# Kernel optimization log

Measured on AMD Instinct MI355X. Metric: run time of the kernel, lower is better.

The kernel has to match this reference:

```python
import jax, jax.numpy as jnp
import numpy as np
import math

NUM_EMBED = 1024
EMBED_DIM = 256
COMMITMENT_COST = 0.25


def setup_inputs() -> dict:
    key = jax.random.key(0)
    k1, k2 = jax.random.split(key)
    inputs = jax.random.normal(k1, (16, EMBED_DIM, 4096), dtype=jnp.float32)
    embed = jax.random.normal(k2, (NUM_EMBED, EMBED_DIM), dtype=jnp.float32)
    return {"inputs": inputs, "embed": embed}


def reference(inputs, embed):
    sg = jax.lax.stop_gradient
    num_embed = embed.shape[0]
    # channels-first (B, D, T) -> (B, T, D)
    x = jnp.swapaxes(inputs, 1, -1)
    B, T, D = x.shape
    flat = x.reshape(-1, D)  # (N, D)
    # pairwise squared distances to the codebook: (N, K)
    d2 = (jnp.sum(flat * flat, axis=1, keepdims=True)
          + jnp.sum(embed * embed, axis=1)
          - 2.0 * flat @ embed.T)
    q_idx = jnp.argmin(d2, axis=1)  # (N,) int
    # one-hot @ embed is just a gather of the nearest codewords
    z_q = embed[q_idx].reshape(x.shape)  # (B, T, D)
    vq_loss = jnp.mean((z_q - sg(x)) ** 2)
    commitment_loss = jnp.mean((sg(z_q) - x) ** 2)
    loss = vq_loss + COMMITMENT_COST * commitment_loss
    # straight-through estimator
    z_q_st = x + sg(z_q - x)
    # codebook usage stats: probs = mean of the one-hot rows
    n = flat.shape[0]
    probs = jnp.zeros((num_embed,), dtype=flat.dtype).at[q_idx].add(1.0) / n
    perplexity = jnp.exp(-jnp.sum(probs * jnp.log(probs + 1e-10)))
    num_spatial_positions = n / B  # == T
    kldiv_r = (math.log(num_embed) * num_spatial_positions
               * jnp.ones((B, 1), dtype=x.dtype))
    z_q_out = jnp.swapaxes(z_q_st, 1, -1)  # back to (B, D, T)
    return z_q_out, loss, kldiv_r, perplexity
```

## Files before the change

### kernel.cpp

```cpp
#include <hip/hip_runtime.h>
#include <math.h>

#define T_DIM 4096
#define D_DIM 256
#define K_NUM 1024
#define B_NUM 16
#define N_TOT (B_NUM * T_DIM)
#define EPS_FLAG 0.25f

typedef float f32x4 __attribute__((ext_vector_type(4)));
typedef _Float16 half8 __attribute__((ext_vector_type(8)));

#define WS_FLAGCNT 0
#define WS_LOSS 4
#define WS_DONE 8
#define WS_HIST 64
#define WS_E2 4352
#define WS_QIDX 8704
#define WS_FLAGLIST 270848
#define WS_BESTD 532992
#define WS_ESWZ 795136
#define WS_ET4 1319424
#define WS_XROWS_ET 2368000
#define WS_XROWS_NOET 1319424

__device__ inline unsigned umin_(unsigned a, unsigned b) { return a < b ? a : b; }
__device__ inline unsigned umax_(unsigned a, unsigned b) { return a > b ? a : b; }

__global__ __launch_bounds__(256) void prep_kernel(const float* __restrict__ embed,
                                                   unsigned char* __restrict__ eswz,
                                                   float* __restrict__ e2,
                                                   float4* __restrict__ eT4, int useET,
                                                   int* __restrict__ wszero) {
    const int tid = threadIdx.x;
    if (blockIdx.x == 0) {
        #pragma unroll
        for (int i = tid; i < 1040; i += 256) wszero[i] = 0;
    }
    const int col = blockIdx.x * 8 + (tid >> 5);
    const int c = tid & 31;
    const float* src = embed + (size_t)col * D_DIM + c * 8;
    half8 h;
    float f[8];
    float s = 0.f;
    #pragma unroll
    for (int j = 0; j < 8; ++j) {
        float v = src[j];
        f[j] = v;
        h[j] = (_Float16)v;
        s = fmaf(v, v, s);
    }
    const int g = col >> 4;
    const int k = c >> 2;
    const int l = ((c & 3) << 4) | (col & 15);
    *(half8*)(eswz + (size_t)g * 8192 + k * 1024 + l * 16) = h;
    if (useET) {
        float4 a = {f[0], f[1], f[2], f[3]};
        float4 b = {f[4], f[5], f[6], f[7]};
        eT4[(size_t)(c * 2 + 0) * K_NUM + col] = a;
        eT4[(size_t)(c * 2 + 1) * K_NUM + col] = b;
    }
    #pragma unroll
    for (int off = 16; off; off >>= 1) s += __shfl_down(s, off);
    if ((tid & 31) == 0) e2[col] = s;
}

#define LOADB(BUF, P) do {                                                        \
    const unsigned char* _bp = eswz + (size_t)(P) * 8192 + (size_t)(l * 16);      \
    _Pragma("unroll")                                                             \
    for (int _k = 0; _k < 8; ++_k) BUF[_k] = *(const half8*)(_bp + _k * 1024);    \
} while (0)

#define PHASE(BUF, P) do {                                                                     \
    const float _bias = fmaf(e2s[(P) * 16 + (l & 15)], -0.5f, -1024.f);                        \
    f32x4 c0e = {_bias, _bias, _bias, _bias};                                                  \
    f32x4 c1e = {_bias, _bias, _bias, _bias};                                                  \
    f32x4 c0o = {0.f, 0.f, 0.f, 0.f};                                                          \
    f32x4 c1o = {0.f, 0.f, 0.f, 0.f};                                                          \
    c0e = __builtin_amdgcn_mfma_f32_16x16x32_f16(Ah[0][0], BUF[0], c0e, 0, 0, 0);              \
    c1e = __builtin_amdgcn_mfma_f32_16x16x32_f16(Ah[1][0], BUF[0], c1e, 0, 0, 0);              \
    c0o = __builtin_amdgcn_mfma_f32_16x16x32_f16(Ah[0][1], BUF[1], c0o, 0, 0, 0);              \
    c1o = __builtin_amdgcn_mfma_f32_16x16x32_f16(Ah[1][1], BUF[1], c1o, 0, 0, 0);              \
    c0e = __builtin_amdgcn_mfma_f32_16x16x32_f16(Ah[0][2], BUF[2], c0e, 0, 0, 0);              \
    c1e = __builtin_amdgcn_mfma_f32_16x16x32_f16(Ah[1][2], BUF[2], c1e, 0, 0, 0);              \
    c0o = __builtin_amdgcn_mfma_f32_16x16x32_f16(Ah[0][3], BUF[3], c0o, 0, 0, 0);              \
    c1o = __builtin_amdgcn_mfma_f32_16x16x32_f16(Ah[1][3], BUF[3], c1o, 0, 0, 0);              \
    c0e = __builtin_amdgcn_mfma_f32_16x16x32_f16(Ah[0][4], BUF[4], c0e, 0, 0, 0);              \
    c1e = __builtin_amdgcn_mfma_f32_16x16x32_f16(Ah[1][4], BUF[4], c1e, 0, 0, 0);              \
    c0o = __builtin_amdgcn_mfma_f32_16x16x32_f16(Ah[0][5], BUF[5], c0o, 0, 0, 0);              \
    c1o = __builtin_amdgcn_mfma_f32_16x16x32_f16(Ah[1][5], BUF[5], c1o, 0, 0, 0);              \
    c0e = __builtin_amdgcn_mfma_f32_16x16x32_f16(Ah[0][6], BUF[6], c0e, 0, 0, 0);              \
    c1e = __builtin_amdgcn_mfma_f32_16x16x32_f16(Ah[1][6], BUF[6], c1e, 0, 0, 0);              \
    c0o = __builtin_amdgcn_mfma_f32_16x16x32_f16(Ah[0][7], BUF[7], c0o, 0, 0, 0);              \
    c1o = __builtin_amdgcn_mfma_f32_16x16x32_f16(Ah[1][7], BUF[7], c1o, 0, 0, 0);              \
    const unsigned _tag = (unsigned)(P);                                                       \
    _Pragma("unroll")                                                                          \
    for (int _r = 0; _r < 4; ++_r) {                                                           \
        float d0v = (c0e[_r] + c0o[_r]) * -2.f;                                                \
        float d1v = (c1e[_r] + c1o[_r]) * -2.f;                                                \
        unsigned k0 = (__float_as_uint(d0v) & 0xFFFFFFC0u) | _tag;                             \
        unsigned k1 = (__float_as_uint(d1v) & 0xFFFFFFC0u) | _tag;                             \
        unsigned m0 = umax_(bestk[_r], k0);                                                    \
        bestk[_r] = umin_(bestk[_r], k0);                                                      \
        seck[_r] = umin_(seck[_r], m0);                                                        \
        unsigned m1 = umax_(bestk[4 + _r], k1);                                                \
        bestk[4 + _r] = umin_(bestk[4 + _r], k1);                                              \
        seck[4 + _r] = umin_(seck[4 + _r], m1);                                                \
    }                                                                                          \
} while (0)

__global__ __launch_bounds__(256, 2) void argmin_mfma_kernel(
    const float* __restrict__ x, const unsigned char* __restrict__ eswz,
    const float* __restrict__ e2, const float* __restrict__ embed,
    int* __restrict__ qidx, int* __restrict__ flagcnt, int* __restrict__ flaglist,
    float* __restrict__ bestd, float* __restrict__ xrows,
    float* __restrict__ out, int* __restrict__ hist,
    float* __restrict__ loss_sum, int cap)
{
    __shared__ float e2s[K_NUM];
    __shared__ __align__(16) float tile[64 * 128];
    __shared__ int   qid_lds[128];
    __shared__ int   lrows[128];
    __shared__ float lbest[128];
    __shared__ int   lcnt;
    __shared__ int   gbase;

    const int tid = threadIdx.x;
    const int w = tid >> 6;
    const int l = tid & 63;
    const int rb = blockIdx.x * 128;
    const int b = rb >> 12;
    const float* xb = x + (size_t)b * (D_DIM * T_DIM);
    if (tid == 0) lcnt = 0;

    half8 B0[8], B1[8];
    LOADB(B0, 0);

    for (int i = tid; i < K_NUM; i += 256) e2s[i] = e2[i];

    half8 Ah[2][8];
    float x2v[2];
    #pragma unroll
    for (int f = 0; f < 2; ++f) {
        const int row = rb + w * 32 + f * 16 + (l & 15);
        const int t = row & (T_DIM - 1);
        const float* xp = xb + t;
        float s2 = 0.f;
        #pragma unroll
        for (int k = 0; k < 8; ++k) {
            const int d0 = k * 32 + ((l >> 4) << 3);
            half8 h;
            #pragma unroll
            for (int j = 0; j < 8; ++j) {
                float v = xp[(size_t)(d0 + j) * T_DIM];
                h[j] = (_Float16)v;
                s2 = fmaf(v, v, s2);
            }
            Ah[f][k] = h;
        }
        x2v[f] = s2;
    }
    #pragma unroll
    for (int f = 0; f < 2; ++f) {
        x2v[f] += __shfl_xor(x2v[f], 16);
        x2v[f] += __shfl_xor(x2v[f], 32);
    }
    __syncthreads();

    unsigned bestk[8], seck[8];
    #pragma unroll
    for (int s = 0; s < 8; ++s) { bestk[s] = 0xFFFFFFFFu; seck[s] = 0xFFFFFFFFu; }

    for (int pp = 0; pp < 31; ++pp) {
        LOADB(B1, 2 * pp + 1);
        PHASE(B0, 2 * pp);
        LOADB(B0, 2 * pp + 2);
        PHASE(B1, 2 * pp + 1);
    }
    LOADB(B1, 63);
    PHASE(B0, 62);
    PHASE(B1, 63);

    float lossw = 0.f;
    #pragma unroll
    for (int slot = 0; slot < 8; ++slot) {
        float bv = __uint_as_float(bestk[slot] & 0xFFFFFFC0u) - 2048.f;
        float sv = __uint_as_float(seck[slot] & 0xFFFFFFC0u) - 2048.f;
        int bi = (int)(bestk[slot] & 63u) * 16 + (l & 15);
        #pragma unroll
        for (int d = 1; d < 16; d <<= 1) {
            float ob = __shfl_xor(bv, d);
            int   oi = __shfl_xor(bi, d);
            float os = __shfl_xor(sv, d);
            bool take = (ob < bv) || (ob == bv && oi < bi);
            float loser = take ? bv : ob;
            bv = take ? ob : bv;
            bi = take ? oi : bi;
            sv = fminf(fminf(sv, os), loser);
        }
        const int srcl = ((l >> 4) << 2) + (slot & 3);
        const float x2r = __shfl(x2v[slot >> 2], srcl);
        if ((l & 15) == 0) {
            const int rloc = w * 32 + (slot >> 2) * 16 + (l >> 4) * 4 + (slot & 3);
            qidx[rb + rloc] = bi;
            qid_lds[rloc] = bi;
            atomicAdd(&hist[bi], 1);
            lossw += bv + x2r;
            if (sv - bv < EPS_FLAG) {
                int lp = atomicAdd(&lcnt, 1);
                lrows[lp] = rb + rloc;
                lbest[lp] = bv;
            }
        }
    }
    lossw += __shfl_down(lossw, 16);
    lossw += __shfl_down(lossw, 32);
    if (l == 0) atomicAdd(loss_sum, lossw);

    __syncthreads();
    const int nloc = lcnt;
    if (tid == 0) gbase = nloc ? atomicAdd(flagcnt, nloc) : 0;
    __syncthreads();
    for (int i = w; i < nloc; i += 4) {
        const int row = lrows[i];
        const int p = gbase + i;
        const bool have = (p < cap);
        if (have) {
            const float* xp = xb + (row & (T_DIM - 1));
            float4 vv;
            vv.x = xp[(size_t)(l * 4 + 0) * T_DIM];
            vv.y = xp[(size_t)(l * 4 + 1) * T_DIM];
            vv.z = xp[(size_t)(l * 4 + 2) * T_DIM];
            vv.w = xp[(size_t)(l * 4 + 3) * T_DIM];
            *(float4*)(xrows + (size_t)p * D_DIM + l * 4) = vv;
        }
        if (l == 0) {
            flaglist[p] = have ? row : (row | 0x80000000);
            bestd[p] = lbest[i];
        }
    }

    const int t0 = rb & (T_DIM - 1);
    float* outb = out + (size_t)b * (D_DIM * T_DIM);
    for (int c = 0; c < 4; ++c) {
        const int d0 = c * 64;
        __syncthreads();
        {
            const int r = tid & 127;
            const int half = tid >> 7;
            const int qi = qid_lds[r];
            const float4* ep = (const float4*)(embed + (size_t)qi * D_DIM + d0 + half * 32);
            #pragma unroll
            for (int i = 0; i < 8; ++i) {
                const float4 ev = ep[i];
                const int dl = half * 32 + i * 4;
                tile[(dl + 0) * 128 + r] = ev.x;
                tile[(dl + 1) * 128 + r] = ev.y;
                tile[(dl + 2) * 128 + r] = ev.z;
                tile[(dl + 3) * 128 + r] = ev.w;
            }
        }
        __syncthreads();
        #pragma unroll 4
        for (int j = 0; j < 32; ++j) {
            const int flat = j * 256 + tid;
            const int dl = flat >> 7;
            const int rr = flat & 127;
            outb[(size_t)(d0 + dl) * T_DIM + t0 + rr] = tile[dl * 128 + rr];
        }
    }
}

__global__ __launch_bounds__(256) void cleanup_kernel(
    const float* __restrict__ x, const float* __restrict__ xrows,
    const float* __restrict__ embed, const float4* __restrict__ eT4, int useET,
    const float* __restrict__ e2,
    const int* __restrict__ flagcnt, const int* __restrict__ flaglist,
    int* __restrict__ qidx, const float* __restrict__ bestd,
    float* __restrict__ loss_sum, float* __restrict__ out, int* __restrict__ hist,
    int* __restrict__ donecnt)
{
    __shared__ float xr[8][256];
    __shared__ float rvall[8][256];
    __shared__ int   rixall[8][256];
    __shared__ int   rowss[8];
    __shared__ int   amlast;
    const int tid = threadIdx.x;
    const int w = tid >> 6;
    int cnt = flagcnt[0];
    if (cnt > N_TOT) cnt = N_TOT;
    for (int base = blockIdx.x * 8; base < cnt; base += gridDim.x * 8) {
        const int nr = (cnt - base < 8) ? (cnt - base) : 8;
        __syncthreads();
        if (tid < 8) rowss[tid] = (tid < nr) ? flaglist[base + tid] : 0;
        __syncthreads();
        #pragma unroll
        for (int r = 0; r < 8; ++r) {
            float v = 0.f;
            if (r < nr) {
                const int fe = rowss[r];
                if (fe >= 0) {
                    v = xrows[(size_t)(base + r) * D_DIM + tid];
                } else {
                    const int row = fe & 0x7FFFFFFF;
                    v = x[(size_t)(row >> 12) * (D_DIM * T_DIM) + (size_t)tid * T_DIM
                          + (row & (T_DIM - 1))];
                }
            }
            xr[r][tid] = v;
        }
        __syncthreads();

        float acc[4][8];
        #pragma unroll
        for (int q = 0; q < 4; ++q)
            #pragma unroll
            for (int r = 0; r < 8; ++r) acc[q][r] = 0.f;
        #pragma unroll 2
        for (int dd4 = 0; dd4 < 64; ++dd4) {
            float4 ev[4];
            #pragma unroll
            for (int q = 0; q < 4; ++q) {
                const int c = q * 256 + tid;
                ev[q] = useET ? eT4[(size_t)dd4 * K_NUM + c]
                              : *((const float4*)(embed + (size_t)c * D_DIM) + dd4);
            }
            float4 xv[8];
            #pragma unroll
            for (int r = 0; r < 8; ++r) xv[r] = *(const float4*)&xr[r][dd4 * 4];
            #pragma unroll
            for (int q = 0; q < 4; ++q) {
                #pragma unroll
                for (int r = 0; r < 8; ++r) {
                    acc[q][r] = fmaf(ev[q].x, xv[r].x, acc[q][r]);
                    acc[q][r] = fmaf(ev[q].y, xv[r].y, acc[q][r]);
                    acc[q][r] = fmaf(ev[q].z, xv[r].z, acc[q][r]);
                    acc[q][r] = fmaf(ev[q].w, xv[r].w, acc[q][r]);
                }
            }
        }
        float bv[8]; int bix[8];
        #pragma unroll
        for (int r = 0; r < 8; ++r) { bv[r] = 3.4e38f; bix[r] = 0x7FFFFFFF; }
        #pragma unroll
        for (int q = 0; q < 4; ++q) {
            const int c = q * 256 + tid;
            const float ec = e2[c];
            #pragma unroll
            for (int r = 0; r < 8; ++r) {
                const float s = fmaf(-2.f, acc[q][r], ec);
                if (s < bv[r] || (s == bv[r] && c < bix[r])) { bv[r] = s; bix[r] = c; }
            }
        }
        #pragma unroll
        for (int r = 0; r < 8; ++r) { rvall[r][tid] = bv[r]; rixall[r][tid] = bix[r]; }
        __syncthreads();
        const int ll = tid & 63;
        #pragma unroll
        for (int rr2 = 0; rr2 < 2; ++rr2) {
            const int r = w * 2 + rr2;
            float mv = 3.4e38f; int mi = 0x7FFFFFFF;
            #pragma unroll
            for (int j = 0; j < 4; ++j) {
                const float v = rvall[r][ll + j * 64];
                const int i2 = rixall[r][ll + j * 64];
                if (v < mv || (v == mv && i2 < mi)) { mv = v; mi = i2; }
            }
            #pragma unroll
            for (int d = 1; d < 64; d <<= 1) {
                const float ov = __shfl_xor(mv, d);
                const int   oi = __shfl_xor(mi, d);
                if (ov < mv || (ov == mv && oi < mi)) { mv = ov; mi = oi; }
            }
            if (r < nr) {
                const int row = rowss[r] & 0x7FFFFFFF;
                const int old = qidx[row];
                if (mi != old) {
                    const int b2 = row >> 12, t2 = row & (T_DIM - 1);
                    const float4 ev = *(const float4*)(embed + (size_t)mi * D_DIM + ll * 4);
                    float* op = out + (size_t)b2 * (D_DIM * T_DIM) + t2;
                    op[(size_t)(ll * 4 + 0) * T_DIM] = ev.x;
                    op[(size_t)(ll * 4 + 1) * T_DIM] = ev.y;
                    op[(size_t)(ll * 4 + 2) * T_DIM] = ev.z;
                    op[(size_t)(ll * 4 + 3) * T_DIM] = ev.w;
                    if (ll == 0) {
                        qidx[row] = mi;
                        atomicAdd(&hist[mi], 1);
                        atomicAdd(&hist[old], -1);
                    }
                }
                if (ll == 0) atomicAdd(loss_sum, mv - bestd[base + r]);
            }
        }
    }

    __threadfence();
    if (tid == 0) {
        const int old = atomicAdd(donecnt, 1);
        amlast = (old == (int)gridDim.x - 1) ? 1 : 0;
    }
    __syncthreads();
    if (amlast) {
        float acc = 0.f;
        for (int i = tid; i < K_NUM; i += 256) {
            const int h = __hip_atomic_load(&hist[i], __ATOMIC_RELAXED,
                                            __HIP_MEMORY_SCOPE_AGENT);
            const float p = (float)h * (1.f / (float)N_TOT);
            acc += p * logf(p + 1e-10f);
        }
        #pragma unroll
        for (int off = 32; off; off >>= 1) acc += __shfl_down(acc, off);
        __shared__ float ls[4];
        if ((tid & 63) == 0) ls[tid >> 6] = acc;
        __syncthreads();
        if (tid == 0) {
            const float H = -(ls[0] + ls[1] + ls[2] + ls[3]);
            const float L = __hip_atomic_load(loss_sum, __ATOMIC_RELAXED,
                                              __HIP_MEMORY_SCOPE_AGENT);
            const size_t base = (size_t)N_TOT * D_DIM;
            out[base] = 1.25f * L * (1.f / 16777216.f);
            const float kld = (float)(6.931471805599453 * 4096.0);
            #pragma unroll
            for (int i = 0; i < 16; ++i) out[base + 1 + i] = kld;
            out[base + 17] = expf(H);
        }
    }
}

extern "C" void kernel_launch(void* const* d_in, const int* in_sizes, int n_in,
                              void* d_out, int out_size, void* d_ws, size_t ws_size,
                              hipStream_t stream)
{
    const float* x     = (const float*)d_in[0];
    const float* embed = (const float*)d_in[1];
    float* out = (float*)d_out;

    char* ws = (char*)d_ws;
    int*   flagcnt  = (int*)(ws + WS_FLAGCNT);
    float* loss_sum = (float*)(ws + WS_LOSS);
    int*   donecnt  = (int*)(ws + WS_DONE);
    int*   hist     = (int*)(ws + WS_HIST);
    float* e2       = (float*)(ws + WS_E2);
    int*   qidx     = (int*)(ws + WS_QIDX);
    int*   flaglist = (int*)(ws + WS_FLAGLIST);
    float* bestd    = (float*)(ws + WS_BESTD);
    unsigned char* eswz = (unsigned char*)(ws + WS_ESWZ);
    float4* eT4     = (float4*)(ws + WS_ET4);

    const int useET = (ws_size >= (size_t)WS_XROWS_ET + 2048) ? 1 : 0;
    const size_t xrows_off = useET ? (size_t)WS_XROWS_ET : (size_t)WS_XROWS_NOET;
    float* xrows = (float*)(ws + xrows_off);

    int cap = 0;
    if (ws_size > xrows_off + 1024) {
        size_t c = (ws_size - xrows_off) / 1024;
        cap = (c > (size_t)N_TOT) ? N_TOT : (int)c;
    }

    prep_kernel<<<128, 256, 0, stream>>>(embed, eswz, e2, eT4, useET, (int*)ws);
    argmin_mfma_kernel<<<N_TOT / 128, 256, 0, stream>>>(x, eswz, e2, embed, qidx,
                                                        flagcnt, flaglist, bestd, xrows,
                                                        out, hist, loss_sum, cap);
    cleanup_kernel<<<512, 256, 0, stream>>>(x, xrows, embed, eT4, useET, e2,
                                            flagcnt, flaglist, qidx, bestd,
                                            loss_sum, out, hist, donecnt);
}
```

Measured before the change: 269.2 us.

## Triple-buffer codebook loads, drop the per-distance scaling, add nontemporal x loads and stores

The MFMA argmin loop moves from double to triple buffering of the swizzled codebook fragments, so loads for a phase are issued further ahead of the MFMAs that consume them. The per-element multiply by -2 is removed. The kernel now tracks a maximum of the positive biased dot-product key, and the distance is rebuilt only once after the loop. The input reads and the output stores become nontemporal to reduce cache pollution. The extra 32 VGPRs for the third buffer could cause spills or lower occupancy under launch_bounds(256,2), and ties between equal keys now resolve to the higher tag.

```diff
diff --git a/kernel.cpp b/kernel.cpp
--- a/kernel.cpp
+++ b/kernel.cpp
@@ -72,7 +72,7 @@
 } while (0)
 
 #define PHASE(BUF, P) do {                                                                     \
-    const float _bias = fmaf(e2s[(P) * 16 + (l & 15)], -0.5f, -1024.f);                        \
+    const float _bias = fmaf(e2s[(P) * 16 + (l & 15)], -0.5f, 1024.f);                         \
     f32x4 c0e = {_bias, _bias, _bias, _bias};                                                  \
     f32x4 c1e = {_bias, _bias, _bias, _bias};                                                  \
     f32x4 c0o = {0.f, 0.f, 0.f, 0.f};                                                          \
@@ -96,16 +96,16 @@
     const unsigned _tag = (unsigned)(P);                                                       \
     _Pragma("unroll")                                                                          \
     for (int _r = 0; _r < 4; ++_r) {                                                           \
-        float d0v = (c0e[_r] + c0o[_r]) * -2.f;                                                \
-        float d1v = (c1e[_r] + c1o[_r]) * -2.f;                                                \
-        unsigned k0 = (__float_as_uint(d0v) & 0xFFFFFFC0u) | _tag;                             \
-        unsigned k1 = (__float_as_uint(d1v) & 0xFFFFFFC0u) | _tag;                             \
-        unsigned m0 = umax_(bestk[_r], k0);                                                    \
-        bestk[_r] = umin_(bestk[_r], k0);                                                      \
-        seck[_r] = umin_(seck[_r], m0);                                                        \
-        unsigned m1 = umax_(bestk[4 + _r], k1);                                                \
-        bestk[4 + _r] = umin_(bestk[4 + _r], k1);                                              \
-        seck[4 + _r] = umin_(seck[4 + _r], m1);                                                \
+        float m0v = c0e[_r] + c0o[_r];                                                         \
+        float m1v = c1e[_r] + c1o[_r];                                                         \
+        unsigned k0 = (__float_as_uint(m0v) & 0xFFFFFFC0u) | _tag;                             \
+        unsigned k1 = (__float_as_uint(m1v) & 0xFFFFFFC0u) | _tag;                             \
+        unsigned d0 = umin_(bestk[_r], k0);                                                    \
+        bestk[_r] = umax_(bestk[_r], k0);                                                      \
+        seck[_r] = umax_(seck[_r], d0);                                                        \
+        unsigned d1 = umin_(bestk[4 + _r], k1);                                                \
+        bestk[4 + _r] = umax_(bestk[4 + _r], k1);                                              \
+        seck[4 + _r] = umax_(seck[4 + _r], d1);                                                \
     }                                                                                          \
 } while (0)
 
@@ -133,8 +133,10 @@
     const float* xb = x + (size_t)b * (D_DIM * T_DIM);
     if (tid == 0) lcnt = 0;
 
-    half8 B0[8], B1[8];
+    half8 B0[8], B1[8], B2[8];
     LOADB(B0, 0);
+    LOADB(B1, 1);
+    LOADB(B2, 2);
 
     for (int i = tid; i < K_NUM; i += 256) e2s[i] = e2[i];
 
@@ -152,7 +154,7 @@
             half8 h;
             #pragma unroll
             for (int j = 0; j < 8; ++j) {
-                float v = xp[(size_t)(d0 + j) * T_DIM];
+                float v = __builtin_nontemporal_load(xp + (size_t)(d0 + j) * T_DIM);
                 h[j] = (_Float16)v;
                 s2 = fmaf(v, v, s2);
             }
@@ -169,23 +171,25 @@
 
     unsigned bestk[8], seck[8];
     #pragma unroll
-    for (int s = 0; s < 8; ++s) { bestk[s] = 0xFFFFFFFFu; seck[s] = 0xFFFFFFFFu; }
-
-    for (int pp = 0; pp < 31; ++pp) {
-        LOADB(B1, 2 * pp + 1);
-        PHASE(B0, 2 * pp);
-        LOADB(B0, 2 * pp + 2);
-        PHASE(B1, 2 * pp + 1);
-    }
-    LOADB(B1, 63);
-    PHASE(B0, 62);
-    PHASE(B1, 63);
+    for (int s = 0; s < 8; ++s) { bestk[s] = 0u; seck[s] = 0u; }
+
+    for (int pp = 0; pp < 20; ++pp) {
+        PHASE(B0, 3 * pp);     LOADB(B0, 3 * pp + 3);
+        PHASE(B1, 3 * pp + 1); LOADB(B1, 3 * pp + 4);
+        PHASE(B2, 3 * pp + 2); LOADB(B2, 3 * pp + 5);
+    }
+    PHASE(B0, 60); LOADB(B0, 63);
+    PHASE(B1, 61);
+    PHASE(B2, 62);
+    PHASE(B0, 63);
 
     float lossw = 0.f;
     #pragma unroll
     for (int slot = 0; slot < 8; ++slot) {
-        float bv = __uint_as_float(bestk[slot] & 0xFFFFFFC0u) - 2048.f;
-        float sv = __uint_as_float(seck[slot] & 0xFFFFFFC0u) - 2048.f;
+        const float mBf = __uint_as_float(bestk[slot] & 0xFFFFFFC0u);
+        const float mSf = __uint_as_float(seck[slot] & 0xFFFFFFC0u);
+        float bv = fmaf(-2.f, mBf, 2048.f);
+        float sv = fmaf(-2.f, mSf, 2048.f);
         int bi = (int)(bestk[slot] & 63u) * 16 + (l & 15);
         #pragma unroll
         for (int d = 1; d < 16; d <<= 1) {
@@ -266,7 +270,8 @@
             const int flat = j * 256 + tid;
             const int dl = flat >> 7;
             const int rr = flat & 127;
-            outb[(size_t)(d0 + dl) * T_DIM + t0 + rr] = tile[dl * 128 + rr];
+            __builtin_nontemporal_store(tile[dl * 128 + rr],
+                                        &outb[(size_t)(d0 + dl) * T_DIM + t0 + rr]);
         }
     }
 }
```

Result: slower. 286.9 us (+6.6%).

## Halve rows per wave in argmin kernel, raise occupancy, flip to max-key tracking

Applied to the files above, without the earlier changes.

Each wave now handles 16 rows instead of 32, so the block covers 64 rows and the grid doubles, while launch bounds ask for 4 blocks per CU instead of 2. The distance is rewritten as a positive score (1024 + x·e − e2/2) and tracked with unsigned max, removing the per-element multiply by -2 and half the accumulator and best/second registers. Codebook B-fragments are preloaded one phase further ahead. This lowers register pressure to gain occupancy and latency hiding, at the cost of loading the codebook from L2 twice as often per row.

```diff
diff --git a/kernel.cpp b/kernel.cpp
--- a/kernel.cpp
+++ b/kernel.cpp
@@ -72,44 +72,29 @@
 } while (0)
 
 #define PHASE(BUF, P) do {                                                                     \
-    const float _bias = fmaf(e2s[(P) * 16 + (l & 15)], -0.5f, -1024.f);                        \
-    f32x4 c0e = {_bias, _bias, _bias, _bias};                                                  \
-    f32x4 c1e = {_bias, _bias, _bias, _bias};                                                  \
-    f32x4 c0o = {0.f, 0.f, 0.f, 0.f};                                                          \
-    f32x4 c1o = {0.f, 0.f, 0.f, 0.f};                                                          \
-    c0e = __builtin_amdgcn_mfma_f32_16x16x32_f16(Ah[0][0], BUF[0], c0e, 0, 0, 0);              \
-    c1e = __builtin_amdgcn_mfma_f32_16x16x32_f16(Ah[1][0], BUF[0], c1e, 0, 0, 0);              \
-    c0o = __builtin_amdgcn_mfma_f32_16x16x32_f16(Ah[0][1], BUF[1], c0o, 0, 0, 0);              \
-    c1o = __builtin_amdgcn_mfma_f32_16x16x32_f16(Ah[1][1], BUF[1], c1o, 0, 0, 0);              \
-    c0e = __builtin_amdgcn_mfma_f32_16x16x32_f16(Ah[0][2], BUF[2], c0e, 0, 0, 0);              \
-    c1e = __builtin_amdgcn_mfma_f32_16x16x32_f16(Ah[1][2], BUF[2], c1e, 0, 0, 0);              \
-    c0o = __builtin_amdgcn_mfma_f32_16x16x32_f16(Ah[0][3], BUF[3], c0o, 0, 0, 0);              \
-    c1o = __builtin_amdgcn_mfma_f32_16x16x32_f16(Ah[1][3], BUF[3], c1o, 0, 0, 0);              \
-    c0e = __builtin_amdgcn_mfma_f32_16x16x32_f16(Ah[0][4], BUF[4], c0e, 0, 0, 0);              \
-    c1e = __builtin_amdgcn_mfma_f32_16x16x32_f16(Ah[1][4], BUF[4], c1e, 0, 0, 0);              \
-    c0o = __builtin_amdgcn_mfma_f32_16x16x32_f16(Ah[0][5], BUF[5], c0o, 0, 0, 0);              \
-    c1o = __builtin_amdgcn_mfma_f32_16x16x32_f16(Ah[1][5], BUF[5], c1o, 0, 0, 0);              \
-    c0e = __builtin_amdgcn_mfma_f32_16x16x32_f16(Ah[0][6], BUF[6], c0e, 0, 0, 0);              \
-    c1e = __builtin_amdgcn_mfma_f32_16x16x32_f16(Ah[1][6], BUF[6], c1e, 0, 0, 0);              \
-    c0o = __builtin_amdgcn_mfma_f32_16x16x32_f16(Ah[0][7], BUF[7], c0o, 0, 0, 0);              \
-    c1o = __builtin_amdgcn_mfma_f32_16x16x32_f16(Ah[1][7], BUF[7], c1o, 0, 0, 0);              \
+    const float _bias = fmaf(e2s[(P) * 16 + (l & 15)], -0.5f, 1024.f);                         \
+    f32x4 ce = {_bias, _bias, _bias, _bias};                                                   \
+    f32x4 co = {0.f, 0.f, 0.f, 0.f};                                                          \
+    ce = __builtin_amdgcn_mfma_f32_16x16x32_f16(Ah[0], BUF[0], ce, 0, 0, 0);                   \
+    co = __builtin_amdgcn_mfma_f32_16x16x32_f16(Ah[1], BUF[1], co, 0, 0, 0);                   \
+    ce = __builtin_amdgcn_mfma_f32_16x16x32_f16(Ah[2], BUF[2], ce, 0, 0, 0);                   \
+    co = __builtin_amdgcn_mfma_f32_16x16x32_f16(Ah[3], BUF[3], co, 0, 0, 0);                   \
+    ce = __builtin_amdgcn_mfma_f32_16x16x32_f16(Ah[4], BUF[4], ce, 0, 0, 0);                   \
+    co = __builtin_amdgcn_mfma_f32_16x16x32_f16(Ah[5], BUF[5], co, 0, 0, 0);                   \
+    ce = __builtin_amdgcn_mfma_f32_16x16x32_f16(Ah[6], BUF[6], ce, 0, 0, 0);                   \
+    co = __builtin_amdgcn_mfma_f32_16x16x32_f16(Ah[7], BUF[7], co, 0, 0, 0);                   \
     const unsigned _tag = (unsigned)(P);                                                       \
     _Pragma("unroll")                                                                          \
     for (int _r = 0; _r < 4; ++_r) {                                                           \
-        float d0v = (c0e[_r] + c0o[_r]) * -2.f;                                                \
-        float d1v = (c1e[_r] + c1o[_r]) * -2.f;                                                \
-        unsigned k0 = (__float_as_uint(d0v) & 0xFFFFFFC0u) | _tag;                             \
-        unsigned k1 = (__float_as_uint(d1v) & 0xFFFFFFC0u) | _tag;                             \
-        unsigned m0 = umax_(bestk[_r], k0);                                                    \
-        bestk[_r] = umin_(bestk[_r], k0);                                                      \
-        seck[_r] = umin_(seck[_r], m0);                                                        \
-        unsigned m1 = umax_(bestk[4 + _r], k1);                                                \
-        bestk[4 + _r] = umin_(bestk[4 + _r], k1);                                              \
-        seck[4 + _r] = umin_(seck[4 + _r], m1);                                                \
+        float mv = ce[_r] + co[_r];                                                            \
+        unsigned kk = (__float_as_uint(mv) & 0xFFFFFFC0u) | _tag;                              \
+        unsigned dd = umin_(bestk[_r], kk);                                                    \
+        bestk[_r] = umax_(bestk[_r], kk);                                                      \
+        seck[_r] = umax_(seck[_r], dd);                                                        \
     }                                                                                          \
 } while (0)
 
-__global__ __launch_bounds__(256, 2) void argmin_mfma_kernel(
+__global__ __launch_bounds__(256, 4) void argmin_mfma_kernel(
     const float* __restrict__ x, const unsigned char* __restrict__ eswz,
     const float* __restrict__ e2, const float* __restrict__ embed,
     int* __restrict__ qidx, int* __restrict__ flagcnt, int* __restrict__ flaglist,
@@ -118,31 +103,31 @@
     float* __restrict__ loss_sum, int cap)
 {
     __shared__ float e2s[K_NUM];
-    __shared__ __align__(16) float tile[64 * 128];
-    __shared__ int   qid_lds[128];
-    __shared__ int   lrows[128];
-    __shared__ float lbest[128];
+    __shared__ __align__(16) float tile[64 * 64];
+    __shared__ int   qid_lds[64];
+    __shared__ int   lrows[64];
+    __shared__ float lbest[64];
     __shared__ int   lcnt;
     __shared__ int   gbase;
 
     const int tid = threadIdx.x;
     const int w = tid >> 6;
     const int l = tid & 63;
-    const int rb = blockIdx.x * 128;
+    const int rb = blockIdx.x * 64;
     const int b = rb >> 12;
     const float* xb = x + (size_t)b * (D_DIM * T_DIM);
     if (tid == 0) lcnt = 0;
 
     half8 B0[8], B1[8];
     LOADB(B0, 0);
+    LOADB(B1, 1);
 
     for (int i = tid; i < K_NUM; i += 256) e2s[i] = e2[i];
 
-    half8 Ah[2][8];
-    float x2v[2];
-    #pragma unroll
-    for (int f = 0; f < 2; ++f) {
-        const int row = rb + w * 32 + f * 16 + (l & 15);
+    half8 Ah[8];
+    float x2v;
+    {
+        const int row = rb + w * 16 + (l & 15);
         const int t = row & (T_DIM - 1);
         const float* xp = xb + t;
         float s2 = 0.f;
@@ -156,36 +141,32 @@
                 h[j] = (_Float16)v;
                 s2 = fmaf(v, v, s2);
             }
-            Ah[f][k] = h;
-        }
-        x2v[f] = s2;
-    }
+            Ah[k] = h;
+        }
+        x2v = s2;
+    }
+    x2v += __shfl_xor(x2v, 16);
+    x2v += __shfl_xor(x2v, 32);
+    __syncthreads();
+
+    unsigned bestk[4], seck[4];
     #pragma unroll
-    for (int f = 0; f < 2; ++f) {
-        x2v[f] += __shfl_xor(x2v[f], 16);
-        x2v[f] += __shfl_xor(x2v[f], 32);
-    }
-    __syncthreads();
-
-    unsigned bestk[8], seck[8];
-    #pragma unroll
-    for (int s = 0; s < 8; ++s) { bestk[s] = 0xFFFFFFFFu; seck[s] = 0xFFFFFFFFu; }
+    for (int s = 0; s < 4; ++s) { bestk[s] = 0u; seck[s] = 0u; }
 
     for (int pp = 0; pp < 31; ++pp) {
-        LOADB(B1, 2 * pp + 1);
-        PHASE(B0, 2 * pp);
-        LOADB(B0, 2 * pp + 2);
-        PHASE(B1, 2 * pp + 1);
-    }
-    LOADB(B1, 63);
+        PHASE(B0, 2 * pp);     LOADB(B0, 2 * pp + 2);
+        PHASE(B1, 2 * pp + 1); LOADB(B1, 2 * pp + 3);
+    }
     PHASE(B0, 62);
     PHASE(B1, 63);
 
     float lossw = 0.f;
     #pragma unroll
-    for (int slot = 0; slot < 8; ++slot) {
-        float bv = __uint_as_float(bestk[slot] & 0xFFFFFFC0u) - 2048.f;
-        float sv = __uint_as_float(seck[slot] & 0xFFFFFFC0u) - 2048.f;
+    for (int slot = 0; slot < 4; ++slot) {
+        const float mBf = __uint_as_float(bestk[slot] & 0xFFFFFFC0u);
+        const float mSf = __uint_as_float(seck[slot] & 0xFFFFFFC0u);
+        float bv = fmaf(-2.f, mBf, 2048.f);
+        float sv = fmaf(-2.f, mSf, 2048.f);
         int bi = (int)(bestk[slot] & 63u) * 16 + (l & 15);
         #pragma unroll
         for (int d = 1; d < 16; d <<= 1) {
@@ -198,10 +179,10 @@
             bi = take ? oi : bi;
             sv = fminf(fminf(sv, os), loser);
         }
-        const int srcl = ((l >> 4) << 2) + (slot & 3);
-        const float x2r = __shfl(x2v[slot >> 2], srcl);
+        const int srcl = ((l >> 4) << 2) + slot;
+        const float x2r = __shfl(x2v, srcl);
         if ((l & 15) == 0) {
-            const int rloc = w * 32 + (slot >> 2) * 16 + (l >> 4) * 4 + (slot & 3);
+            const int rloc = w * 16 + (l >> 4) * 4 + slot;
             qidx[rb + rloc] = bi;
             qid_lds[rloc] = bi;
             atomicAdd(&hist[bi], 1);
@@ -246,27 +227,27 @@
         const int d0 = c * 64;
         __syncthreads();
         {
-            const int r = tid & 127;
-            const int half = tid >> 7;
+            const int r = tid & 63;
+            const int q = tid >> 6;
             const int qi = qid_lds[r];
-            const float4* ep = (const float4*)(embed + (size_t)qi * D_DIM + d0 + half * 32);
-            #pragma unroll
-            for (int i = 0; i < 8; ++i) {
+            const float4* ep = (const float4*)(embed + (size_t)qi * D_DIM + d0 + q * 16);
+            #pragma unroll
+            for (int i = 0; i < 4; ++i) {
                 const float4 ev = ep[i];
-                const int dl = half * 32 + i * 4;
-                tile[(dl + 0) * 128 + r] = ev.x;
-                tile[(dl + 1) * 128 + r] = ev.y;
-                tile[(dl + 2) * 128 + r] = ev.z;
-                tile[(dl + 3) * 128 + r] = ev.w;
+                const int dl = q * 16 + i * 4;
+                tile[(dl + 0) * 64 + r] = ev.x;
+                tile[(dl + 1) * 64 + r] = ev.y;
+                tile[(dl + 2) * 64 + r] = ev.z;
+                tile[(dl + 3) * 64 + r] = ev.w;
             }
         }
         __syncthreads();
         #pragma unroll 4
-        for (int j = 0; j < 32; ++j) {
+        for (int j = 0; j < 16; ++j) {
             const int flat = j * 256 + tid;
-            const int dl = flat >> 7;
-            const int rr = flat & 127;
-            outb[(size_t)(d0 + dl) * T_DIM + t0 + rr] = tile[dl * 128 + rr];
+            const int dl = flat >> 6;
+            const int rr = flat & 63;
+            outb[(size_t)(d0 + dl) * T_DIM + t0 + rr] = tile[dl * 64 + rr];
         }
     }
 }
@@ -458,9 +439,9 @@
     }
 
     prep_kernel<<<128, 256, 0, stream>>>(embed, eswz, e2, eT4, useET, (int*)ws);
-    argmin_mfma_kernel<<<N_TOT / 128, 256, 0, stream>>>(x, eswz, e2, embed, qidx,
-                                                        flagcnt, flaglist, bestd, xrows,
-                                                        out, hist, loss_sum, cap);
+    argmin_mfma_kernel<<<N_TOT / 64, 256, 0, stream>>>(x, eswz, e2, embed, qidx,
+                                                       flagcnt, flaglist, bestd, xrows,
+                                                       out, hist, loss_sum, cap);
     cleanup_kernel<<<512, 256, 0, stream>>>(x, xrows, embed, eT4, useET, e2,
                                             flagcnt, flaglist, qidx, bestd,
                                             loss_sum, out, hist, donecnt);
```

Result: slower. 301.2 us (+11.9%).

## Fuse fp32 recheck of ambiguous rows and finalization into argmin kernel

Applied to the files above, without the earlier changes.

When the transposed codebook fits in the workspace, each argmin block now re-scores its own near-tie rows in exact fp32 right away, one row at a time with a block reduction. It patches qidx, the histogram and the loss in place, and the last block to finish computes the perplexity and loss outputs. This drops the separate cleanup kernel launch and the round trip through the global flag list. The catch is that the per-row recheck is serialized inside each block with many syncthreads, and it runs before the output write, so a block with many flagged rows now takes longer. The fallback cleanup kernel's loop order is also restructured.

```diff
diff --git a/kernel.cpp b/kernel.cpp
--- a/kernel.cpp
+++ b/kernel.cpp
@@ -112,18 +112,23 @@
 __global__ __launch_bounds__(256, 2) void argmin_mfma_kernel(
     const float* __restrict__ x, const unsigned char* __restrict__ eswz,
     const float* __restrict__ e2, const float* __restrict__ embed,
+    const float4* __restrict__ eT4, int useET,
     int* __restrict__ qidx, int* __restrict__ flagcnt, int* __restrict__ flaglist,
     float* __restrict__ bestd, float* __restrict__ xrows,
     float* __restrict__ out, int* __restrict__ hist,
-    float* __restrict__ loss_sum, int cap)
+    float* __restrict__ loss_sum, int cap, int* __restrict__ donecnt)
 {
     __shared__ float e2s[K_NUM];
     __shared__ __align__(16) float tile[64 * 128];
     __shared__ int   qid_lds[128];
     __shared__ int   lrows[128];
     __shared__ float lbest[128];
+    __shared__ __align__(16) float xs[256];
+    __shared__ float rv[256];
+    __shared__ int   rix[256];
     __shared__ int   lcnt;
     __shared__ int   gbase;
+    __shared__ int   amlast;
 
     const int tid = threadIdx.x;
     const int w = tid >> 6;
@@ -208,7 +213,7 @@
             lossw += bv + x2r;
             if (sv - bv < EPS_FLAG) {
                 int lp = atomicAdd(&lcnt, 1);
-                lrows[lp] = rb + rloc;
+                lrows[lp] = rloc;
                 lbest[lp] = bv;
             }
         }
@@ -219,24 +224,77 @@
 
     __syncthreads();
     const int nloc = lcnt;
-    if (tid == 0) gbase = nloc ? atomicAdd(flagcnt, nloc) : 0;
-    __syncthreads();
-    for (int i = w; i < nloc; i += 4) {
-        const int row = lrows[i];
-        const int p = gbase + i;
-        const bool have = (p < cap);
-        if (have) {
-            const float* xp = xb + (row & (T_DIM - 1));
-            float4 vv;
-            vv.x = xp[(size_t)(l * 4 + 0) * T_DIM];
-            vv.y = xp[(size_t)(l * 4 + 1) * T_DIM];
-            vv.z = xp[(size_t)(l * 4 + 2) * T_DIM];
-            vv.w = xp[(size_t)(l * 4 + 3) * T_DIM];
-            *(float4*)(xrows + (size_t)p * D_DIM + l * 4) = vv;
-        }
-        if (l == 0) {
-            flaglist[p] = have ? row : (row | 0x80000000);
-            bestd[p] = lbest[i];
+
+    if (useET) {
+        for (int i = 0; i < nloc; ++i) {
+            const int rloc = lrows[i];
+            const int row = rb + rloc;
+            const int t = row & (T_DIM - 1);
+            xs[tid] = xb[(size_t)tid * T_DIM + t];
+            __syncthreads();
+            float acc4[4] = {0.f, 0.f, 0.f, 0.f};
+            for (int dd4 = 0; dd4 < 64; ++dd4) {
+                const float4 xv = *(const float4*)&xs[dd4 * 4];
+                #pragma unroll
+                for (int q = 0; q < 4; ++q) {
+                    const float4 ev = eT4[(size_t)dd4 * K_NUM + q * 256 + tid];
+                    acc4[q] = fmaf(ev.x, xv.x, acc4[q]);
+                    acc4[q] = fmaf(ev.y, xv.y, acc4[q]);
+                    acc4[q] = fmaf(ev.z, xv.z, acc4[q]);
+                    acc4[q] = fmaf(ev.w, xv.w, acc4[q]);
+                }
+            }
+            float bvv = 3.4e38f; int bii = 0x7FFFFFFF;
+            #pragma unroll
+            for (int q = 0; q < 4; ++q) {
+                const int c = q * 256 + tid;
+                const float s = fmaf(-2.f, acc4[q], e2s[c]);
+                if (s < bvv || (s == bvv && c < bii)) { bvv = s; bii = c; }
+            }
+            rv[tid] = bvv; rix[tid] = bii;
+            __syncthreads();
+            for (int off = 128; off; off >>= 1) {
+                if (tid < off) {
+                    const float ov = rv[tid + off]; const int oi = rix[tid + off];
+                    if (ov < rv[tid] || (ov == rv[tid] && oi < rix[tid])) {
+                        rv[tid] = ov; rix[tid] = oi;
+                    }
+                }
+                __syncthreads();
+            }
+            if (tid == 0) {
+                const int mi = rix[0];
+                const int old = qid_lds[rloc];
+                if (mi != old) {
+                    qid_lds[rloc] = mi;
+                    qidx[row] = mi;
+                    atomicAdd(&hist[mi], 1);
+                    atomicAdd(&hist[old], -1);
+                }
+                atomicAdd(loss_sum, rv[0] - lbest[i]);
+            }
+            __syncthreads();
+        }
+    } else {
+        if (tid == 0) gbase = nloc ? atomicAdd(flagcnt, nloc) : 0;
+        __syncthreads();
+        for (int i = w; i < nloc; i += 4) {
+            const int row = rb + lrows[i];
+            const int p = gbase + i;
+            const bool have = (p < cap);
+            if (have) {
+                const float* xp = xb + (row & (T_DIM - 1));
+                float4 vv;
+                vv.x = xp[(size_t)(l * 4 + 0) * T_DIM];
+                vv.y = xp[(size_t)(l * 4 + 1) * T_DIM];
+                vv.z = xp[(size_t)(l * 4 + 2) * T_DIM];
+                vv.w = xp[(size_t)(l * 4 + 3) * T_DIM];
+                *(float4*)(xrows + (size_t)p * D_DIM + l * 4) = vv;
+            }
+            if (l == 0) {
+                flaglist[p] = have ? row : (row | 0x80000000);
+                bestd[p] = lbest[i];
+            }
         }
     }
 
@@ -269,12 +327,44 @@
             outb[(size_t)(d0 + dl) * T_DIM + t0 + rr] = tile[dl * 128 + rr];
         }
     }
+
+    if (useET) {
+        __threadfence();
+        if (tid == 0) {
+            const int old = atomicAdd(donecnt, 1);
+            amlast = (old == (int)gridDim.x - 1) ? 1 : 0;
+        }
+        __syncthreads();
+        if (amlast) {
+            float acc = 0.f;
+            for (int i = tid; i < K_NUM; i += 256) {
+                const int h = __hip_atomic_load(&hist[i], __ATOMIC_RELAXED,
+                                                __HIP_MEMORY_SCOPE_AGENT);
+                const float p = (float)h * (1.f / (float)N_TOT);
+                acc += p * logf(p + 1e-10f);
+            }
+            #pragma unroll
+            for (int off = 32; off; off >>= 1) acc += __shfl_down(acc, off);
+            if ((tid & 63) == 0) rv[tid >> 6] = acc;
+            __syncthreads();
+            if (tid == 0) {
+                const float H = -(rv[0] + rv[1] + rv[2] + rv[3]);
+                const float L = __hip_atomic_load(loss_sum, __ATOMIC_RELAXED,
+                                                  __HIP_MEMORY_SCOPE_AGENT);
+                const size_t base = (size_t)N_TOT * D_DIM;
+                out[base] = 1.25f * L * (1.f / 16777216.f);
+                const float kld = (float)(6.931471805599453 * 4096.0);
+                #pragma unroll
+                for (int i = 0; i < 16; ++i) out[base + 1 + i] = kld;
+                out[base + 17] = expf(H);
+            }
+        }
+    }
 }
 
 __global__ __launch_bounds__(256) void cleanup_kernel(
     const float* __restrict__ x, const float* __restrict__ xrows,
-    const float* __restrict__ embed, const float4* __restrict__ eT4, int useET,
-    const float* __restrict__ e2,
+    const float* __restrict__ embed, const float* __restrict__ e2,
     const int* __restrict__ flagcnt, const int* __restrict__ flaglist,
     int* __restrict__ qidx, const float* __restrict__ bestd,
     float* __restrict__ loss_sum, float* __restrict__ out, int* __restrict__ hist,
@@ -311,44 +401,31 @@
         }
         __syncthreads();
 
-        float acc[4][8];
-        #pragma unroll
-        for (int q = 0; q < 4; ++q)
-            #pragma unroll
-            for (int r = 0; r < 8; ++r) acc[q][r] = 0.f;
-        #pragma unroll 2
-        for (int dd4 = 0; dd4 < 64; ++dd4) {
-            float4 ev[4];
-            #pragma unroll
-            for (int q = 0; q < 4; ++q) {
-                const int c = q * 256 + tid;
-                ev[q] = useET ? eT4[(size_t)dd4 * K_NUM + c]
-                              : *((const float4*)(embed + (size_t)c * D_DIM) + dd4);
-            }
-            float4 xv[8];
-            #pragma unroll
-            for (int r = 0; r < 8; ++r) xv[r] = *(const float4*)&xr[r][dd4 * 4];
-            #pragma unroll
-            for (int q = 0; q < 4; ++q) {
+        float bv[8]; int bix[8];
+        #pragma unroll
+        for (int r = 0; r < 8; ++r) { bv[r] = 3.4e38f; bix[r] = 0x7FFFFFFF; }
+        for (int q = 0; q < 4; ++q) {
+            const int c = q * 256 + tid;
+            const float4* ep = (const float4*)(embed + (size_t)c * D_DIM);
+            float acc[8];
+            #pragma unroll
+            for (int r = 0; r < 8; ++r) acc[r] = 0.f;
+            #pragma unroll 8
+            for (int dd = 0; dd < 64; ++dd) {
+                const float4 ev = ep[dd];
                 #pragma unroll
                 for (int r = 0; r < 8; ++r) {
-                    acc[q][r] = fmaf(ev[q].x, xv[r].x, acc[q][r]);
-                    acc[q][r] = fmaf(ev[q].y, xv[r].y, acc[q][r]);
-                    acc[q][r] = fmaf(ev[q].z, xv[r].z, acc[q][r]);
-                    acc[q][r] = fmaf(ev[q].w, xv[r].w, acc[q][r]);
+                    const float4 xv = *(const float4*)&xr[r][dd * 4];
+                    acc[r] = fmaf(ev.x, xv.x, acc[r]);
+                    acc[r] = fmaf(ev.y, xv.y, acc[r]);
+                    acc[r] = fmaf(ev.z, xv.z, acc[r]);
+                    acc[r] = fmaf(ev.w, xv.w, acc[r]);
                 }
             }
-        }
-        float bv[8]; int bix[8];
-        #pragma unroll
-        for (int r = 0; r < 8; ++r) { bv[r] = 3.4e38f; bix[r] = 0x7FFFFFFF; }
-        #pragma unroll
-        for (int q = 0; q < 4; ++q) {
-            const int c = q * 256 + tid;
             const float ec = e2[c];
             #pragma unroll
             for (int r = 0; r < 8; ++r) {
-                const float s = fmaf(-2.f, acc[q][r], ec);
+                const float s = fmaf(-2.f, acc[r], ec);
                 if (s < bv[r] || (s == bv[r] && c < bix[r])) { bv[r] = s; bix[r] = c; }
             }
         }
@@ -447,7 +524,7 @@
     unsigned char* eswz = (unsigned char*)(ws + WS_ESWZ);
     float4* eT4     = (float4*)(ws + WS_ET4);
 
-    const int useET = (ws_size >= (size_t)WS_XROWS_ET + 2048) ? 1 : 0;
+    const int useET = (ws_size >= (size_t)WS_ET4 + 1048576 + 2048) ? 1 : 0;
     const size_t xrows_off = useET ? (size_t)WS_XROWS_ET : (size_t)WS_XROWS_NOET;
     float* xrows = (float*)(ws + xrows_off);
 
@@ -458,10 +535,12 @@
     }
 
     prep_kernel<<<128, 256, 0, stream>>>(embed, eswz, e2, eT4, useET, (int*)ws);
-    argmin_mfma_kernel<<<N_TOT / 128, 256, 0, stream>>>(x, eswz, e2, embed, qidx,
-                                                        flagcnt, flaglist, bestd, xrows,
-                                                        out, hist, loss_sum, cap);
-    cleanup_kernel<<<512, 256, 0, stream>>>(x, xrows, embed, eT4, useET, e2,
-                                            flagcnt, flaglist, qidx, bestd,
-                                            loss_sum, out, hist, donecnt);
+    argmin_mfma_kernel<<<N_TOT / 128, 256, 0, stream>>>(x, eswz, e2, embed, eT4, useET,
+                                                        qidx, flagcnt, flaglist, bestd,
+                                                        xrows, out, hist, loss_sum, cap,
+                                                        donecnt);
+    if (!useET) {
+        cleanup_kernel<<<512, 256, 0, stream>>>(x, xrows, embed, e2, flagcnt, flaglist,
+                                                qidx, bestd, loss_sum, out, hist, donecnt);
+    }
 }
```

Result: slower. 341.6 us (+26.9%).
